# Optimization experiments

Measured on AMD Instinct MI355X. Metric: run time of the kernel, lower is better.

Reference implementation:

```python
import jax, jax.numpy as jnp
import numpy as np

B, HR, WR, C, HEADS, WS = 32, 64, 64, 128, 4, 8
HD = C // HEADS            # head dim = 32
N = WS * WS                # tokens per window = 64
NB = (2 * WS - 1) ** 2     # relative-bias table rows = 225
EPS = 1e-5


def _relative_bias_index():
    # Static int index, identical to SwinMSA._get_relative_bias_index
    coords = np.stack(np.meshgrid(np.arange(WS), np.arange(WS), indexing='ij'))  # (2, ws, ws)
    flat = coords.reshape(2, -1)                      # (2, n)
    rel = flat[:, :, None] - flat[:, None, :]         # (2, n, n)
    rel = rel.transpose(1, 2, 0).copy()               # (n, n, 2)
    rel[:, :, 0] += WS - 1
    rel[:, :, 1] += WS - 1
    rel[:, :, 0] *= 2 * WS - 1
    return rel.sum(-1)                                # (n, n) int

_REL_IDX = _relative_bias_index()


def _ln(x, g, b):
    m = jnp.mean(x, axis=-1, keepdims=True)
    v = jnp.mean(jnp.square(x - m), axis=-1, keepdims=True)
    return (x - m) * jax.lax.rsqrt(v + EPS) * g + b


def setup_inputs() -> dict:
    key = jax.random.key(0)
    ks = jax.random.split(key, 16)
    s = 0.02
    return {
        'x': jax.random.normal(ks[0], (B, HR * WR, C), jnp.float32),
        'qkv_w': jax.random.normal(ks[1], (C, 3 * C), jnp.float32) * s,
        'qkv_b': jnp.zeros((3 * C,), jnp.float32),
        'proj_w': jax.random.normal(ks[2], (C, C), jnp.float32) * s,
        'proj_b': jnp.zeros((C,), jnp.float32),
        'rel_bias_table': jax.random.normal(ks[3], (NB, HEADS), jnp.float32) * s,
        'ln1_g': jnp.ones((C,), jnp.float32),
        'ln1_b': jnp.zeros((C,), jnp.float32),
        'ln2_g': jnp.ones((C,), jnp.float32),
        'ln2_b': jnp.zeros((C,), jnp.float32),
        'mlp_w1': jax.random.normal(ks[4], (C, 4 * C), jnp.float32) * s,
        'mlp_b1': jnp.zeros((4 * C,), jnp.float32),
        'mlp_w2': jax.random.normal(ks[5], (4 * C, C), jnp.float32) * s,
        'mlp_b2': jnp.zeros((C,), jnp.float32),
    }


def reference(x, qkv_w, qkv_b, proj_w, proj_b, rel_bias_table,
              ln1_g, ln1_b, ln2_g, ln2_b, mlp_w1, mlp_b1, mlp_w2, mlp_b2):
    b = x.shape[0]
    hb, wb = HR // WS, WR // WS
    img = x.reshape(b, HR, WR, C)
    n1 = _ln(img, ln1_g, ln1_b)
    # window_partition: '(wy h) (wx w)' split puts window coord OUTER (strided windows),
    # faithful to the source rearrange.
    part = n1.reshape(b, WS, hb, WS, wb, C).transpose(0, 2, 4, 1, 3, 5)
    part = part.reshape(b * hb * wb, N, C)            # (Bw, n, c)
    qkv = part @ qkv_w + qkv_b                        # (Bw, n, 3c)
    # rearrange 'b n (h d c) -> d b n h c': channel factors as (head, 3, head_dim)
    qkv = qkv.reshape(-1, N, HEADS, 3, HD)
    q, k, v = qkv[..., 0, :], qkv[..., 1, :], qkv[..., 2, :]   # (Bw, n, h, hd)
    energy = jnp.einsum('bqhe,bkhe->bqhk', q, k) * (HD ** -0.5)
    bias = rel_bias_table[_REL_IDX.reshape(-1)].reshape(N, N, HEADS)
    bias = bias.transpose(2, 0, 1)                    # (h, n, n)
    energy = energy + bias.transpose(1, 0, 2)[None]   # broadcast as (q, h, k)
    attn = jax.nn.softmax(energy, axis=-1)
    out = jnp.einsum('bihv,bvhd->bihd', attn, v).reshape(-1, N, C)
    out = out @ proj_w + proj_b                       # (Bw, n, c)
    # window_reverse (inverse of the strided partition)
    rev = out.reshape(b, hb, wb, WS, WS, C).transpose(0, 3, 1, 4, 2, 5)
    rev = rev.reshape(b, HR * WR, C)
    msa = x + rev
    h2 = _ln(msa, ln2_g, ln2_b)
    mlp = jax.nn.gelu(h2 @ mlp_w1 + mlp_b1, approximate=False) @ mlp_w2 + mlp_b2
    return msa + mlp
```

## Files before the change

### kernel.cpp

```cpp
#include <hip/hip_runtime.h>
#include <hip/hip_bf16.h>
#include <hip/hip_fp16.h>

typedef __attribute__((ext_vector_type(4))) float f32x4;
typedef __attribute__((ext_vector_type(8))) short bf16x8;
typedef __attribute__((ext_vector_type(4))) short bf16x4;
typedef unsigned short u16;
typedef unsigned char u8;

__device__ __forceinline__ short fbf(float f){
  __hip_bfloat16 h = __float2bfloat16(f);
  return *reinterpret_cast<short*>(&h);
}
__device__ __forceinline__ float bf2f(short s){
  return __uint_as_float(((unsigned)(unsigned short)s) << 16);
}
__device__ __forceinline__ unsigned f2e5(float v){
  __half h = __float2half(v);
  unsigned hu = (unsigned)*reinterpret_cast<unsigned short*>(&h);
  hu = hu + 0x7Fu + ((hu >> 8) & 1u);
  return (hu >> 8) & 0xFFu;
}
__device__ __forceinline__ float e52f(unsigned b){
  unsigned short hb = (unsigned short)(b << 8);
  __half h = *reinterpret_cast<__half*>(&hb);
  return __half2float(h);
}

#define LOG2E 1.4426950408889634f

__global__ void repack_kernel(const float* __restrict__ qkv_w, const float* __restrict__ proj_w,
                              const float* __restrict__ w1, const float* __restrict__ w2,
                              const float* __restrict__ tbl,
                              u16* __restrict__ rq, u16* __restrict__ rp,
                              u16* __restrict__ r1, u16* __restrict__ r2,
                              float* __restrict__ be){
  const int i = blockIdx.x * 256 + threadIdx.x;
  const int j = i & 7, lane = (i >> 3) & 63, f = i >> 9;
  const int kr = (lane >> 4) * 8 + j;
  const int c16 = lane & 15;
  if (i < 49152){ int nt = f % 24, kk = f / 24; rq[i] = (u16)fbf(qkv_w[(kk*32 + kr)*384 + nt*16 + c16]); }
  if (i < 16384){ int nt = f & 7,  kk = f >> 3; rp[i] = (u16)fbf(proj_w[(kk*32 + kr)*128 + nt*16 + c16]); }
  if (i < 65536){ int nt = f & 31, kk = f >> 5; r1[i] = (u16)fbf(w1[(kk*32 + kr)*512 + nt*16 + c16]); }
  if (i < 65536){ int nt = f & 7,  kk = f >> 3; r2[i] = (u16)fbf(w2[(kk*32 + kr)*128 + nt*16 + c16]); }
  if (i < 16384){
    int rg = i & 3, ln = (i >> 2) & 63, g = i >> 8;
    int nt = g & 3, mt = (g >> 2) & 3, h = g >> 4;
    int row = mt*16 + (ln >> 4)*4 + rg;
    int col = nt*16 + (ln & 15);
    int rel = ((col >> 3) - (row >> 3) + 7) * 15 + ((col & 7) - (row & 7) + 7);
    be[i] = tbl[rel*4 + h] * LOG2E;
  }
}

__global__ __launch_bounds__(256, 3)
void block_kernel(const float* __restrict__ x,
                  const float* __restrict__ qkv_b, const float* __restrict__ proj_b,
                  const float* __restrict__ ln1_g, const float* __restrict__ ln1_b,
                  const float* __restrict__ ln2_g, const float* __restrict__ ln2_b,
                  const u16* __restrict__ rep_qkv, const u16* __restrict__ rep_proj,
                  const u16* __restrict__ rep_w1, const u16* __restrict__ rep_w2,
                  const float* __restrict__ mlp_b1, const float* __restrict__ mlp_b2,
                  const float* __restrict__ bias_exp,
                  float* __restrict__ out){
  __shared__ __align__(16) u16 smem[20480];
  u16* sLN = smem;
  u16* sQ  = smem;
  u16* sK  = smem + 8192;
  u16* sP  = smem;
  u16* sO  = smem;
  u16* stg = smem + 8192;
  u16* sH  = smem;
  u16* sG  = smem + 16384;
  u8*  sVe5 = (u8*)(smem + 16384);

  const int tid = threadIdx.x, lane = tid & 63, wid = tid >> 6;
  const int wdw = blockIdx.x;
  const int bb = wdw >> 6, ihb = (wdw >> 3) & 7, iwb = wdw & 7;
  const float* xb = x + (size_t)bb * 4096 * 128;
  float* ob = out + (size_t)bb * 4096 * 128;
  const f32x4 z4 = {0.f, 0.f, 0.f, 0.f};
  const int rb = tid >> 4, cb = tid & 15, c0g = cb * 8;
  const int r15 = lane & 15, kg = lane >> 4;

  {
    float g8[8], b8[8];
    *(f32x4*)&g8[0] = *(const f32x4*)(ln1_g + c0g);
    *(f32x4*)&g8[4] = *(const f32x4*)(ln1_g + c0g + 4);
    *(f32x4*)&b8[0] = *(const f32x4*)(ln1_b + c0g);
    *(f32x4*)&b8[4] = *(const f32x4*)(ln1_b + c0g + 4);
    #pragma unroll
    for (int it = 0; it < 4; ++it){
      const int r = it * 16 + rb;
      const int pix = ((r >> 3) * 8 + ihb) * 64 + (r & 7) * 8 + iwb;
      float fl[8];
      *(f32x4*)&fl[0] = *(const f32x4*)(xb + (size_t)pix * 128 + c0g);
      *(f32x4*)&fl[4] = *(const f32x4*)(xb + (size_t)pix * 128 + c0g + 4);
      float s = 0.f, sq = 0.f;
      #pragma unroll
      for (int j = 0; j < 8; ++j){ s += fl[j]; sq += fl[j]*fl[j]; }
      #pragma unroll
      for (int m = 1; m < 16; m <<= 1){ s += __shfl_xor(s, m); sq += __shfl_xor(sq, m); }
      const float mean = s * (1.f/128.f);
      const float rs = __builtin_amdgcn_rsqf(sq * (1.f/128.f) - mean*mean + 1e-5f);
      bf16x8 o;
      #pragma unroll
      for (int j = 0; j < 8; ++j) o[j] = fbf((fl[j]-mean)*rs*g8[j] + b8[j]);
      *(bf16x8*)&sLN[r*128 + (c0g ^ ((r & 7) << 3))] = o;
    }
  }
  __syncthreads();

  {
    f32x4 aqk[4][4];
    f32x4 av[4][2];
    #pragma unroll
    for (int ct = 0; ct < 4; ++ct){
      const f32x4 bq = *(const f32x4*)(qkv_b + wid*96 + ct*16 + kg*4);
      #pragma unroll
      for (int tt = 0; tt < 4; ++tt) aqk[ct][tt] = bq;
    }
    #pragma unroll
    for (int nt = 0; nt < 2; ++nt){
      const float bv = qkv_b[wid*96 + 64 + nt*16 + r15];
      const f32x4 bv4 = {bv, bv, bv, bv};
      #pragma unroll
      for (int mt = 0; mt < 4; ++mt) av[mt][nt] = bv4;
    }
    #pragma unroll
    for (int kk = 0; kk < 4; ++kk){
      bf16x8 L[4], aW[4], bWv[2];
      const int c0 = kk*32 + kg*8;
      #pragma unroll
      for (int t = 0; t < 4; ++t){
        const int row = t*16 + r15;
        L[t] = *(const bf16x8*)&sLN[row*128 + (c0 ^ ((row & 7) << 3))];
      }
      #pragma unroll
      for (int ct = 0; ct < 4; ++ct)
        aW[ct] = *(const bf16x8*)(rep_qkv + (size_t)((kk*24 + wid*6 + ct)*64 + lane)*8);
      #pragma unroll
      for (int nt = 0; nt < 2; ++nt)
        bWv[nt] = *(const bf16x8*)(rep_qkv + (size_t)((kk*24 + wid*6 + 4 + nt)*64 + lane)*8);
      #pragma unroll
      for (int ct = 0; ct < 4; ++ct)
        #pragma unroll
        for (int tt = 0; tt < 4; ++tt)
          aqk[ct][tt] = __builtin_amdgcn_mfma_f32_16x16x32_bf16(aW[ct], L[tt], aqk[ct][tt], 0, 0, 0);
      #pragma unroll
      for (int mt = 0; mt < 4; ++mt)
        #pragma unroll
        for (int nt = 0; nt < 2; ++nt)
          av[mt][nt] = __builtin_amdgcn_mfma_f32_16x16x32_bf16(L[mt], bWv[nt], av[mt][nt], 0, 0, 0);
    }
    __syncthreads();
    #pragma unroll
    for (int ct = 0; ct < 4; ++ct){
      u16* dst = (ct < 2) ? sQ : sK;
      const float scl = (ct < 2) ? 0.2550348296f : 1.0f;
      const int colu = wid*32 + (ct & 1)*16 + kg*4;
      #pragma unroll
      for (int tt = 0; tt < 4; ++tt){
        const int row = tt*16 + r15;
        bf16x4 pk;
        #pragma unroll
        for (int rg = 0; rg < 4; ++rg) pk[rg] = fbf(aqk[ct][tt][rg] * scl);
        *(bf16x4*)&dst[row*128 + (colu ^ ((row & 7) << 3))] = pk;
      }
    }
    #pragma unroll
    for (int nt = 0; nt < 2; ++nt){
      const int row = wid*32 + nt*16 + r15;
      #pragma unroll
      for (int mt = 0; mt < 4; ++mt){
        const int colu = mt*16 + kg*4;
        unsigned pk = f2e5(av[mt][nt][0]) | (f2e5(av[mt][nt][1]) << 8)
                    | (f2e5(av[mt][nt][2]) << 16) | (f2e5(av[mt][nt][3]) << 24);
        *(unsigned*)(sVe5 + row*64 + (colu ^ ((row & 7) << 3))) = pk;
      }
    }
  }
  __syncthreads();

  f32x4 s4[4][4];
  {
    bf16x8 aK[4], bQ[4];
    #pragma unroll
    for (int t = 0; t < 4; ++t){
      const int row = t*16 + r15;
      const int off = (wid*32 + kg*8) ^ ((row & 7) << 3);
      aK[t] = *(const bf16x8*)&sK[row*128 + off];
      bQ[t] = *(const bf16x8*)&sQ[row*128 + off];
    }
    #pragma unroll
    for (int mtk = 0; mtk < 4; ++mtk)
      #pragma unroll
      for (int ntq = 0; ntq < 4; ++ntq){
        const f32x4 cb4 = *(const f32x4*)(bias_exp + (size_t)(((wid*4 + mtk)*4 + ntq)*64 + lane)*4);
        s4[mtk][ntq] = __builtin_amdgcn_mfma_f32_16x16x32_bf16(aK[mtk], bQ[ntq], cb4, 0, 0, 0);
      }
  }
  #pragma unroll
  for (int ntq = 0; ntq < 4; ++ntq){
    float sum = 0.f;
    #pragma unroll
    for (int mtk = 0; mtk < 4; ++mtk)
      #pragma unroll
      for (int rg = 0; rg < 4; ++rg){
        const float e = __builtin_amdgcn_exp2f(s4[mtk][ntq][rg]);
        s4[mtk][ntq][rg] = e; sum += e;
      }
    sum += __shfl_xor(sum, 16);
    sum += __shfl_xor(sum, 32);
    const float inv = __builtin_amdgcn_rcpf(sum);
    #pragma unroll
    for (int mtk = 0; mtk < 4; ++mtk)
      #pragma unroll
      for (int rg = 0; rg < 4; ++rg) s4[mtk][ntq][rg] *= inv;
  }
  __syncthreads();
  #pragma unroll
  for (int ntq = 0; ntq < 4; ++ntq){
    const int row = ntq*16 + r15;
    #pragma unroll
    for (int mtk = 0; mtk < 4; ++mtk){
      const int colu = mtk*16 + kg*4;
      bf16x4 pk;
      #pragma unroll
      for (int rg = 0; rg < 4; ++rg) pk[rg] = fbf(s4[mtk][ntq][rg]);
      *(bf16x4*)&sP[wid*4096 + row*64 + (colu ^ ((row & 7) << 3))] = pk;
    }
  }

  {
    f32x4 o4[2][4];
    #pragma unroll
    for (int dt = 0; dt < 2; ++dt)
      #pragma unroll
      for (int qt = 0; qt < 4; ++qt) o4[dt][qt] = z4;
    #pragma unroll
    for (int ks = 0; ks < 2; ++ks){
      bf16x8 aV[2], bP[4];
      #pragma unroll
      for (int dt = 0; dt < 2; ++dt){
        const int rowd = wid*32 + dt*16 + r15;
        const u8* pv = sVe5 + rowd*64 + ((ks*32 + kg*8) ^ ((rowd & 7) << 3));
        const unsigned w0 = *(const unsigned*)pv;
        const unsigned w1 = *(const unsigned*)(pv + 4);
        bf16x8 a;
        #pragma unroll
        for (int j = 0; j < 4; ++j){
          a[j]   = fbf(e52f((w0 >> (8*j)) & 0xFFu));
          a[4+j] = fbf(e52f((w1 >> (8*j)) & 0xFFu));
        }
        aV[dt] = a;
      }
      #pragma unroll
      for (int qt = 0; qt < 4; ++qt){
        const int rowq = qt*16 + r15;
        bP[qt] = *(const bf16x8*)&sP[wid*4096 + rowq*64 + ((ks*32 + kg*8) ^ ((rowq & 7) << 3))];
      }
      #pragma unroll
      for (int dt = 0; dt < 2; ++dt)
        #pragma unroll
        for (int qt = 0; qt < 4; ++qt)
          o4[dt][qt] = __builtin_amdgcn_mfma_f32_16x16x32_bf16(aV[dt], bP[qt], o4[dt][qt], 0, 0, 0);
    }
    __syncthreads();
    #pragma unroll
    for (int dt = 0; dt < 2; ++dt){
      const int dbase = wid*32 + dt*16 + kg*4;
      #pragma unroll
      for (int qt = 0; qt < 4; ++qt){
        const int q = qt*16 + r15;
        bf16x4 pk;
        #pragma unroll
        for (int rg = 0; rg < 4; ++rg) pk[rg] = fbf(o4[dt][qt][rg]);
        *(bf16x4*)&sO[q*128 + (dbase ^ ((q & 7) << 3))] = pk;
      }
    }
  }
  __syncthreads();

  {
    f32x4 xv[2][4];
    #pragma unroll
    for (int ot = 0; ot < 2; ++ot){
      const int cbase = (wid*2 + ot)*16 + kg*4;
      #pragma unroll
      for (int tt = 0; tt < 4; ++tt){
        const int tok = tt*16 + r15;
        const int pix = ((tok >> 3) * 8 + ihb) * 64 + (tok & 7) * 8 + iwb;
        xv[ot][tt] = *(const f32x4*)(xb + (size_t)pix * 128 + cbase);
      }
    }
    f32x4 po[2][4];
    #pragma unroll
    for (int ot = 0; ot < 2; ++ot){
      const f32x4 pb4 = *(const f32x4*)(proj_b + (wid*2 + ot)*16 + kg*4);
      #pragma unroll
      for (int tt = 0; tt < 4; ++tt) po[ot][tt] = pb4;
    }
    #pragma unroll
    for (int kk = 0; kk < 4; ++kk){
      bf16x8 aWp[2], bO[4];
      #pragma unroll
      for (int ot = 0; ot < 2; ++ot)
        aWp[ot] = *(const bf16x8*)(rep_proj + (size_t)((kk*8 + wid*2 + ot)*64 + lane)*8);
      #pragma unroll
      for (int tt = 0; tt < 4; ++tt){
        const int row = tt*16 + r15;
        bO[tt] = *(const bf16x8*)&sO[row*128 + ((kk*32 + kg*8) ^ ((row & 7) << 3))];
      }
      #pragma unroll
      for (int ot = 0; ot < 2; ++ot)
        #pragma unroll
        for (int tt = 0; tt < 4; ++tt)
          po[ot][tt] = __builtin_amdgcn_mfma_f32_16x16x32_bf16(aWp[ot], bO[tt], po[ot][tt], 0, 0, 0);
    }
    #pragma unroll
    for (int ot = 0; ot < 2; ++ot){
      const int cbase = (wid*2 + ot)*16 + kg*4;
      #pragma unroll
      for (int tt = 0; tt < 4; ++tt){
        const int tok = tt*16 + r15;
        bf16x4 pk;
        #pragma unroll
        for (int rg = 0; rg < 4; ++rg) pk[rg] = fbf(po[ot][tt][rg] + xv[ot][tt][rg]);
        *(bf16x4*)&stg[tok*128 + (cbase ^ ((tok & 7) << 3))] = pk;
      }
    }
  }
  __syncthreads();

  {
    float g8[8], b8[8];
    *(f32x4*)&g8[0] = *(const f32x4*)(ln2_g + c0g);
    *(f32x4*)&g8[4] = *(const f32x4*)(ln2_g + c0g + 4);
    *(f32x4*)&b8[0] = *(const f32x4*)(ln2_b + c0g);
    *(f32x4*)&b8[4] = *(const f32x4*)(ln2_b + c0g + 4);
    #pragma unroll
    for (int it = 0; it < 4; ++it){
      const int r = it * 16 + rb;
      bf16x8 m8 = *(const bf16x8*)&stg[r*128 + (c0g ^ ((r & 7) << 3))];
      float fl[8];
      #pragma unroll
      for (int j = 0; j < 8; ++j) fl[j] = bf2f(m8[j]);
      float s = 0.f, sq = 0.f;
      #pragma unroll
      for (int j = 0; j < 8; ++j){ s += fl[j]; sq += fl[j]*fl[j]; }
      #pragma unroll
      for (int m = 1; m < 16; m <<= 1){ s += __shfl_xor(s, m); sq += __shfl_xor(sq, m); }
      const float mean = s * (1.f/128.f);
      const float rs = __builtin_amdgcn_rsqf(sq * (1.f/128.f) - mean*mean + 1e-5f);
      bf16x8 o;
      #pragma unroll
      for (int j = 0; j < 8; ++j) o[j] = fbf((fl[j]-mean)*rs*g8[j] + b8[j]);
      *(bf16x8*)&sH[r*128 + (c0g ^ ((r & 7) << 3))] = o;
    }
  }
  __syncthreads();

  f32x4 accO[2][4];
  #pragma unroll
  for (int ot = 0; ot < 2; ++ot){
    const f32x4 b2v = *(const f32x4*)(mlp_b2 + (wid*2 + ot)*16 + kg*4);
    #pragma unroll
    for (int tt = 0; tt < 4; ++tt) accO[ot][tt] = b2v;
  }
  #pragma unroll
  for (int c = 0; c < 8; ++c){
    f32x4 t4[4];
    {
      const f32x4 b1v = *(const f32x4*)(mlp_b1 + c*64 + wid*16 + kg*4);
      #pragma unroll
      for (int tt = 0; tt < 4; ++tt) t4[tt] = b1v;
    }
    #pragma unroll
    for (int kk = 0; kk < 4; ++kk){
      const int c0 = kk*32 + kg*8;
      bf16x8 aW = *(const bf16x8*)(rep_w1 + (size_t)((kk*32 + c*4 + wid)*64 + lane)*8);
      bf16x8 bL[4];
      #pragma unroll
      for (int tt = 0; tt < 4; ++tt){
        const int row = tt*16 + r15;
        bL[tt] = *(const bf16x8*)&sH[row*128 + (c0 ^ ((row & 7) << 3))];
      }
      #pragma unroll
      for (int tt = 0; tt < 4; ++tt)
        t4[tt] = __builtin_amdgcn_mfma_f32_16x16x32_bf16(aW, bL[tt], t4[tt], 0, 0, 0);
    }
    bf16x4 gp[4];
    #pragma unroll
    for (int tt = 0; tt < 4; ++tt){
      #pragma unroll
      for (int rg = 0; rg < 4; ++rg){
        const float v = t4[tt][rg];
        const float e = __builtin_amdgcn_exp2f(-2.4554669f * v);
        gp[tt][rg] = fbf(v * __builtin_amdgcn_rcpf(1.f + e));
      }
    }
    __syncthreads();
    {
      const int colu = wid*16 + kg*4;
      #pragma unroll
      for (int tt = 0; tt < 4; ++tt){
        const int row = tt*16 + r15;
        *(bf16x4*)&sG[row*64 + (colu ^ ((row & 7) << 3))] = gp[tt];
      }
    }
    __syncthreads();
    #pragma unroll
    for (int kk2 = 0; kk2 < 2; ++kk2){
      bf16x8 aW2[2], bG[4];
      const int c0 = kk2*32 + kg*8;
      #pragma unroll
      for (int ot = 0; ot < 2; ++ot)
        aW2[ot] = *(const bf16x8*)(rep_w2 + (size_t)(((c*2 + kk2)*8 + wid*2 + ot)*64 + lane)*8);
      #pragma unroll
      for (int tt = 0; tt < 4; ++tt){
        const int row = tt*16 + r15;
        bG[tt] = *(const bf16x8*)&sG[row*64 + (c0 ^ ((row & 7) << 3))];
      }
      #pragma unroll
      for (int ot = 0; ot < 2; ++ot)
        #pragma unroll
        for (int tt = 0; tt < 4; ++tt)
          accO[ot][tt] = __builtin_amdgcn_mfma_f32_16x16x32_bf16(aW2[ot], bG[tt], accO[ot][tt], 0, 0, 0);
    }
  }

  #pragma unroll
  for (int ot = 0; ot < 2; ++ot){
    const int cbase = (wid*2 + ot)*16 + kg*4;
    #pragma unroll
    for (int tt = 0; tt < 4; ++tt){
      const int tok = tt*16 + r15;
      const int pix = ((tok >> 3) * 8 + ihb) * 64 + (tok & 7) * 8 + iwb;
      bf16x4 m4 = *(const bf16x4*)&stg[tok*128 + (cbase ^ ((tok & 7) << 3))];
      f32x4 o;
      #pragma unroll
      for (int rg = 0; rg < 4; ++rg) o[rg] = bf2f(m4[rg]) + accO[ot][tt][rg];
      *(f32x4*)(ob + (size_t)pix * 128 + cbase) = o;
    }
  }
}

extern "C" void kernel_launch(void* const* d_in, const int* in_sizes, int n_in,
                              void* d_out, int out_size, void* d_ws, size_t ws_size,
                              hipStream_t stream){
  (void)in_sizes; (void)n_in; (void)out_size; (void)ws_size;
  const float* x      = (const float*)d_in[0];
  const float* qkv_w  = (const float*)d_in[1];
  const float* qkv_b  = (const float*)d_in[2];
  const float* proj_w = (const float*)d_in[3];
  const float* proj_b = (const float*)d_in[4];
  const float* tbl    = (const float*)d_in[5];
  const float* ln1_g  = (const float*)d_in[6];
  const float* ln1_b  = (const float*)d_in[7];
  const float* ln2_g  = (const float*)d_in[8];
  const float* ln2_b  = (const float*)d_in[9];
  const float* w1     = (const float*)d_in[10];
  const float* b1     = (const float*)d_in[11];
  const float* w2     = (const float*)d_in[12];
  const float* b2     = (const float*)d_in[13];

  char* ws = (char*)d_ws;
  u16*   rq  = (u16*)ws;
  u16*   rp  = (u16*)(ws + 98304);
  u16*   r1  = (u16*)(ws + 131072);
  u16*   r2  = (u16*)(ws + 262144);
  float* be  = (float*)(ws + 393216);

  hipLaunchKernelGGL(repack_kernel, dim3(256), dim3(256), 0, stream,
                     qkv_w, proj_w, w1, w2, tbl, rq, rp, r1, r2, be);
  hipLaunchKernelGGL(block_kernel, dim3(2048), dim3(256), 0, stream,
                     x, qkv_b, proj_b, ln1_g, ln1_b, ln2_g, ln2_b,
                     rq, rp, r1, r2, b1, b2, be, (float*)d_out);
}
```

Measured before the change: 103.9 us.

## Split each window across eight waves by head and token half

Doubles the block size to 512 threads. Each of the eight waves now handles one head (or output column group) for half of the window's 64 tokens, where before one wave covered a head for all tokens. Per-wave accumulator and fragment arrays are halved, and launch bounds move from (256,3) to (512,2). This cuts register pressure and puts more waves in flight per CU. In exchange, each weight fragment is loaded from global memory by two waves instead of one, and each block synchronises more waves at every barrier.

```diff
diff --git a/kernel.cpp b/kernel.cpp
--- a/kernel.cpp
+++ b/kernel.cpp
@@ -53,7 +53,7 @@
   }
 }
 
-__global__ __launch_bounds__(256, 3)
+__global__ __launch_bounds__(512, 2)
 void block_kernel(const float* __restrict__ x,
                   const float* __restrict__ qkv_b, const float* __restrict__ proj_b,
                   const float* __restrict__ ln1_g, const float* __restrict__ ln1_b,
@@ -74,7 +74,8 @@
   u16* sG  = smem + 16384;
   u8*  sVe5 = (u8*)(smem + 16384);
 
-  const int tid = threadIdx.x, lane = tid & 63, wid = tid >> 6;
+  const int tid = threadIdx.x, lane = tid & 63, wid8 = tid >> 6;
+  const int head = wid8 & 3, half = wid8 >> 2, tb = half * 2;
   const int wdw = blockIdx.x;
   const int bb = wdw >> 6, ihb = (wdw >> 3) & 7, iwb = wdw & 7;
   const float* xb = x + (size_t)bb * 4096 * 128;
@@ -90,8 +91,8 @@
     *(f32x4*)&b8[0] = *(const f32x4*)(ln1_b + c0g);
     *(f32x4*)&b8[4] = *(const f32x4*)(ln1_b + c0g + 4);
     #pragma unroll
-    for (int it = 0; it < 4; ++it){
-      const int r = it * 16 + rb;
+    for (int it = 0; it < 2; ++it){
+      const int r = it * 32 + rb;
       const int pix = ((r >> 3) * 8 + ihb) * 64 + (r & 7) * 8 + iwb;
       float fl[8];
       *(f32x4*)&fl[0] = *(const f32x4*)(xb + (size_t)pix * 128 + c0g);
@@ -112,103 +113,106 @@
   __syncthreads();
 
   {
-    f32x4 aqk[4][4];
-    f32x4 av[4][2];
+    f32x4 aqk[4][2];
+    f32x4 av[2][2];
     #pragma unroll
     for (int ct = 0; ct < 4; ++ct){
-      const f32x4 bq = *(const f32x4*)(qkv_b + wid*96 + ct*16 + kg*4);
-      #pragma unroll
-      for (int tt = 0; tt < 4; ++tt) aqk[ct][tt] = bq;
+      const f32x4 bq = *(const f32x4*)(qkv_b + head*96 + ct*16 + kg*4);
+      #pragma unroll
+      for (int t2 = 0; t2 < 2; ++t2) aqk[ct][t2] = bq;
     }
     #pragma unroll
     for (int nt = 0; nt < 2; ++nt){
-      const float bv = qkv_b[wid*96 + 64 + nt*16 + r15];
+      const float bv = qkv_b[head*96 + 64 + nt*16 + r15];
       const f32x4 bv4 = {bv, bv, bv, bv};
       #pragma unroll
-      for (int mt = 0; mt < 4; ++mt) av[mt][nt] = bv4;
+      for (int t2 = 0; t2 < 2; ++t2) av[t2][nt] = bv4;
     }
     #pragma unroll
     for (int kk = 0; kk < 4; ++kk){
-      bf16x8 L[4], aW[4], bWv[2];
+      bf16x8 L[2], aW[4], bWv[2];
       const int c0 = kk*32 + kg*8;
       #pragma unroll
-      for (int t = 0; t < 4; ++t){
-        const int row = t*16 + r15;
-        L[t] = *(const bf16x8*)&sLN[row*128 + (c0 ^ ((row & 7) << 3))];
+      for (int t2 = 0; t2 < 2; ++t2){
+        const int row = (tb + t2)*16 + r15;
+        L[t2] = *(const bf16x8*)&sLN[row*128 + (c0 ^ ((row & 7) << 3))];
       }
       #pragma unroll
       for (int ct = 0; ct < 4; ++ct)
-        aW[ct] = *(const bf16x8*)(rep_qkv + (size_t)((kk*24 + wid*6 + ct)*64 + lane)*8);
+        aW[ct] = *(const bf16x8*)(rep_qkv + (size_t)((kk*24 + head*6 + ct)*64 + lane)*8);
       #pragma unroll
       for (int nt = 0; nt < 2; ++nt)
-        bWv[nt] = *(const bf16x8*)(rep_qkv + (size_t)((kk*24 + wid*6 + 4 + nt)*64 + lane)*8);
+        bWv[nt] = *(const bf16x8*)(rep_qkv + (size_t)((kk*24 + head*6 + 4 + nt)*64 + lane)*8);
       #pragma unroll
       for (int ct = 0; ct < 4; ++ct)
         #pragma unroll
-        for (int tt = 0; tt < 4; ++tt)
-          aqk[ct][tt] = __builtin_amdgcn_mfma_f32_16x16x32_bf16(aW[ct], L[tt], aqk[ct][tt], 0, 0, 0);
-      #pragma unroll
-      for (int mt = 0; mt < 4; ++mt)
+        for (int t2 = 0; t2 < 2; ++t2)
+          aqk[ct][t2] = __builtin_amdgcn_mfma_f32_16x16x32_bf16(aW[ct], L[t2], aqk[ct][t2], 0, 0, 0);
+      #pragma unroll
+      for (int t2 = 0; t2 < 2; ++t2)
         #pragma unroll
         for (int nt = 0; nt < 2; ++nt)
-          av[mt][nt] = __builtin_amdgcn_mfma_f32_16x16x32_bf16(L[mt], bWv[nt], av[mt][nt], 0, 0, 0);
+          av[t2][nt] = __builtin_amdgcn_mfma_f32_16x16x32_bf16(L[t2], bWv[nt], av[t2][nt], 0, 0, 0);
     }
     __syncthreads();
     #pragma unroll
     for (int ct = 0; ct < 4; ++ct){
       u16* dst = (ct < 2) ? sQ : sK;
       const float scl = (ct < 2) ? 0.2550348296f : 1.0f;
-      const int colu = wid*32 + (ct & 1)*16 + kg*4;
-      #pragma unroll
-      for (int tt = 0; tt < 4; ++tt){
-        const int row = tt*16 + r15;
+      const int colu = head*32 + (ct & 1)*16 + kg*4;
+      #pragma unroll
+      for (int t2 = 0; t2 < 2; ++t2){
+        const int row = (tb + t2)*16 + r15;
         bf16x4 pk;
         #pragma unroll
-        for (int rg = 0; rg < 4; ++rg) pk[rg] = fbf(aqk[ct][tt][rg] * scl);
+        for (int rg = 0; rg < 4; ++rg) pk[rg] = fbf(aqk[ct][t2][rg] * scl);
         *(bf16x4*)&dst[row*128 + (colu ^ ((row & 7) << 3))] = pk;
       }
     }
     #pragma unroll
     for (int nt = 0; nt < 2; ++nt){
-      const int row = wid*32 + nt*16 + r15;
-      #pragma unroll
-      for (int mt = 0; mt < 4; ++mt){
-        const int colu = mt*16 + kg*4;
-        unsigned pk = f2e5(av[mt][nt][0]) | (f2e5(av[mt][nt][1]) << 8)
-                    | (f2e5(av[mt][nt][2]) << 16) | (f2e5(av[mt][nt][3]) << 24);
+      const int row = head*32 + nt*16 + r15;
+      #pragma unroll
+      for (int t2 = 0; t2 < 2; ++t2){
+        const int colu = (tb + t2)*16 + kg*4;
+        unsigned pk = f2e5(av[t2][nt][0]) | (f2e5(av[t2][nt][1]) << 8)
+                    | (f2e5(av[t2][nt][2]) << 16) | (f2e5(av[t2][nt][3]) << 24);
         *(unsigned*)(sVe5 + row*64 + (colu ^ ((row & 7) << 3))) = pk;
       }
     }
   }
   __syncthreads();
 
-  f32x4 s4[4][4];
-  {
-    bf16x8 aK[4], bQ[4];
+  f32x4 s4[4][2];
+  {
+    bf16x8 aK[4], bQ[2];
     #pragma unroll
     for (int t = 0; t < 4; ++t){
       const int row = t*16 + r15;
-      const int off = (wid*32 + kg*8) ^ ((row & 7) << 3);
-      aK[t] = *(const bf16x8*)&sK[row*128 + off];
-      bQ[t] = *(const bf16x8*)&sQ[row*128 + off];
+      aK[t] = *(const bf16x8*)&sK[row*128 + ((head*32 + kg*8) ^ ((row & 7) << 3))];
+    }
+    #pragma unroll
+    for (int q2 = 0; q2 < 2; ++q2){
+      const int row = (tb + q2)*16 + r15;
+      bQ[q2] = *(const bf16x8*)&sQ[row*128 + ((head*32 + kg*8) ^ ((row & 7) << 3))];
     }
     #pragma unroll
     for (int mtk = 0; mtk < 4; ++mtk)
       #pragma unroll
-      for (int ntq = 0; ntq < 4; ++ntq){
-        const f32x4 cb4 = *(const f32x4*)(bias_exp + (size_t)(((wid*4 + mtk)*4 + ntq)*64 + lane)*4);
-        s4[mtk][ntq] = __builtin_amdgcn_mfma_f32_16x16x32_bf16(aK[mtk], bQ[ntq], cb4, 0, 0, 0);
+      for (int q2 = 0; q2 < 2; ++q2){
+        const f32x4 cb4 = *(const f32x4*)(bias_exp + (size_t)(((head*4 + mtk)*4 + tb + q2)*64 + lane)*4);
+        s4[mtk][q2] = __builtin_amdgcn_mfma_f32_16x16x32_bf16(aK[mtk], bQ[q2], cb4, 0, 0, 0);
       }
   }
   #pragma unroll
-  for (int ntq = 0; ntq < 4; ++ntq){
+  for (int q2 = 0; q2 < 2; ++q2){
     float sum = 0.f;
     #pragma unroll
     for (int mtk = 0; mtk < 4; ++mtk)
       #pragma unroll
       for (int rg = 0; rg < 4; ++rg){
-        const float e = __builtin_amdgcn_exp2f(s4[mtk][ntq][rg]);
-        s4[mtk][ntq][rg] = e; sum += e;
+        const float e = __builtin_amdgcn_exp2f(s4[mtk][q2][rg]);
+        s4[mtk][q2][rg] = e; sum += e;
       }
     sum += __shfl_xor(sum, 16);
     sum += __shfl_xor(sum, 32);
@@ -216,34 +220,34 @@
     #pragma unroll
     for (int mtk = 0; mtk < 4; ++mtk)
       #pragma unroll
-      for (int rg = 0; rg < 4; ++rg) s4[mtk][ntq][rg] *= inv;
+      for (int rg = 0; rg < 4; ++rg) s4[mtk][q2][rg] *= inv;
   }
   __syncthreads();
   #pragma unroll
-  for (int ntq = 0; ntq < 4; ++ntq){
-    const int row = ntq*16 + r15;
+  for (int q2 = 0; q2 < 2; ++q2){
+    const int row = (tb + q2)*16 + r15;
     #pragma unroll
     for (int mtk = 0; mtk < 4; ++mtk){
       const int colu = mtk*16 + kg*4;
       bf16x4 pk;
       #pragma unroll
-      for (int rg = 0; rg < 4; ++rg) pk[rg] = fbf(s4[mtk][ntq][rg]);
-      *(bf16x4*)&sP[wid*4096 + row*64 + (colu ^ ((row & 7) << 3))] = pk;
-    }
-  }
-
-  {
-    f32x4 o4[2][4];
+      for (int rg = 0; rg < 4; ++rg) pk[rg] = fbf(s4[mtk][q2][rg]);
+      *(bf16x4*)&sP[head*4096 + row*64 + (colu ^ ((row & 7) << 3))] = pk;
+    }
+  }
+
+  {
+    f32x4 o4[2][2];
     #pragma unroll
     for (int dt = 0; dt < 2; ++dt)
       #pragma unroll
-      for (int qt = 0; qt < 4; ++qt) o4[dt][qt] = z4;
+      for (int q2 = 0; q2 < 2; ++q2) o4[dt][q2] = z4;
     #pragma unroll
     for (int ks = 0; ks < 2; ++ks){
-      bf16x8 aV[2], bP[4];
+      bf16x8 aV[2], bP[2];
       #pragma unroll
       for (int dt = 0; dt < 2; ++dt){
-        const int rowd = wid*32 + dt*16 + r15;
+        const int rowd = head*32 + dt*16 + r15;
         const u8* pv = sVe5 + rowd*64 + ((ks*32 + kg*8) ^ ((rowd & 7) << 3));
         const unsigned w0 = *(const unsigned*)pv;
         const unsigned w1 = *(const unsigned*)(pv + 4);
@@ -256,26 +260,26 @@
         aV[dt] = a;
       }
       #pragma unroll
-      for (int qt = 0; qt < 4; ++qt){
-        const int rowq = qt*16 + r15;
-        bP[qt] = *(const bf16x8*)&sP[wid*4096 + rowq*64 + ((ks*32 + kg*8) ^ ((rowq & 7) << 3))];
+      for (int q2 = 0; q2 < 2; ++q2){
+        const int rowq = (tb + q2)*16 + r15;
+        bP[q2] = *(const bf16x8*)&sP[head*4096 + rowq*64 + ((ks*32 + kg*8) ^ ((rowq & 7) << 3))];
       }
       #pragma unroll
       for (int dt = 0; dt < 2; ++dt)
         #pragma unroll
-        for (int qt = 0; qt < 4; ++qt)
-          o4[dt][qt] = __builtin_amdgcn_mfma_f32_16x16x32_bf16(aV[dt], bP[qt], o4[dt][qt], 0, 0, 0);
+        for (int q2 = 0; q2 < 2; ++q2)
+          o4[dt][q2] = __builtin_amdgcn_mfma_f32_16x16x32_bf16(aV[dt], bP[q2], o4[dt][q2], 0, 0, 0);
     }
     __syncthreads();
     #pragma unroll
     for (int dt = 0; dt < 2; ++dt){
-      const int dbase = wid*32 + dt*16 + kg*4;
-      #pragma unroll
-      for (int qt = 0; qt < 4; ++qt){
-        const int q = qt*16 + r15;
+      const int dbase = head*32 + dt*16 + kg*4;
+      #pragma unroll
+      for (int q2 = 0; q2 < 2; ++q2){
+        const int q = (tb + q2)*16 + r15;
         bf16x4 pk;
         #pragma unroll
-        for (int rg = 0; rg < 4; ++rg) pk[rg] = fbf(o4[dt][qt][rg]);
+        for (int rg = 0; rg < 4; ++rg) pk[rg] = fbf(o4[dt][q2][rg]);
         *(bf16x4*)&sO[q*128 + (dbase ^ ((q & 7) << 3))] = pk;
       }
     }
@@ -283,50 +287,50 @@
   __syncthreads();
 
   {
-    f32x4 xv[2][4];
+    f32x4 xv[2][2];
     #pragma unroll
     for (int ot = 0; ot < 2; ++ot){
-      const int cbase = (wid*2 + ot)*16 + kg*4;
-      #pragma unroll
-      for (int tt = 0; tt < 4; ++tt){
-        const int tok = tt*16 + r15;
+      const int cbase = (head*2 + ot)*16 + kg*4;
+      #pragma unroll
+      for (int t2 = 0; t2 < 2; ++t2){
+        const int tok = (tb + t2)*16 + r15;
         const int pix = ((tok >> 3) * 8 + ihb) * 64 + (tok & 7) * 8 + iwb;
-        xv[ot][tt] = *(const f32x4*)(xb + (size_t)pix * 128 + cbase);
-      }
-    }
-    f32x4 po[2][4];
+        xv[ot][t2] = *(const f32x4*)(xb + (size_t)pix * 128 + cbase);
+      }
+    }
+    f32x4 po[2][2];
     #pragma unroll
     for (int ot = 0; ot < 2; ++ot){
-      const f32x4 pb4 = *(const f32x4*)(proj_b + (wid*2 + ot)*16 + kg*4);
-      #pragma unroll
-      for (int tt = 0; tt < 4; ++tt) po[ot][tt] = pb4;
+      const f32x4 pb4 = *(const f32x4*)(proj_b + (head*2 + ot)*16 + kg*4);
+      #pragma unroll
+      for (int t2 = 0; t2 < 2; ++t2) po[ot][t2] = pb4;
     }
     #pragma unroll
     for (int kk = 0; kk < 4; ++kk){
-      bf16x8 aWp[2], bO[4];
+      bf16x8 aWp[2], bO[2];
       #pragma unroll
       for (int ot = 0; ot < 2; ++ot)
-        aWp[ot] = *(const bf16x8*)(rep_proj + (size_t)((kk*8 + wid*2 + ot)*64 + lane)*8);
-      #pragma unroll
-      for (int tt = 0; tt < 4; ++tt){
-        const int row = tt*16 + r15;
-        bO[tt] = *(const bf16x8*)&sO[row*128 + ((kk*32 + kg*8) ^ ((row & 7) << 3))];
+        aWp[ot] = *(const bf16x8*)(rep_proj + (size_t)((kk*8 + head*2 + ot)*64 + lane)*8);
+      #pragma unroll
+      for (int t2 = 0; t2 < 2; ++t2){
+        const int row = (tb + t2)*16 + r15;
+        bO[t2] = *(const bf16x8*)&sO[row*128 + ((kk*32 + kg*8) ^ ((row & 7) << 3))];
       }
       #pragma unroll
       for (int ot = 0; ot < 2; ++ot)
         #pragma unroll
-        for (int tt = 0; tt < 4; ++tt)
-          po[ot][tt] = __builtin_amdgcn_mfma_f32_16x16x32_bf16(aWp[ot], bO[tt], po[ot][tt], 0, 0, 0);
+        for (int t2 = 0; t2 < 2; ++t2)
+          po[ot][t2] = __builtin_amdgcn_mfma_f32_16x16x32_bf16(aWp[ot], bO[t2], po[ot][t2], 0, 0, 0);
     }
     #pragma unroll
     for (int ot = 0; ot < 2; ++ot){
-      const int cbase = (wid*2 + ot)*16 + kg*4;
-      #pragma unroll
-      for (int tt = 0; tt < 4; ++tt){
-        const int tok = tt*16 + r15;
+      const int cbase = (head*2 + ot)*16 + kg*4;
+      #pragma unroll
+      for (int t2 = 0; t2 < 2; ++t2){
+        const int tok = (tb + t2)*16 + r15;
         bf16x4 pk;
         #pragma unroll
-        for (int rg = 0; rg < 4; ++rg) pk[rg] = fbf(po[ot][tt][rg] + xv[ot][tt][rg]);
+        for (int rg = 0; rg < 4; ++rg) pk[rg] = fbf(po[ot][t2][rg] + xv[ot][t2][rg]);
         *(bf16x4*)&stg[tok*128 + (cbase ^ ((tok & 7) << 3))] = pk;
       }
     }
@@ -340,8 +344,8 @@
     *(f32x4*)&b8[0] = *(const f32x4*)(ln2_b + c0g);
     *(f32x4*)&b8[4] = *(const f32x4*)(ln2_b + c0g + 4);
     #pragma unroll
-    for (int it = 0; it < 4; ++it){
-      const int r = it * 16 + rb;
+    for (int it = 0; it < 2; ++it){
+      const int r = it * 32 + rb;
       bf16x8 m8 = *(const bf16x8*)&stg[r*128 + (c0g ^ ((r & 7) << 3))];
       float fl[8];
       #pragma unroll
@@ -361,86 +365,86 @@
   }
   __syncthreads();
 
-  f32x4 accO[2][4];
+  f32x4 accO[2][2];
   #pragma unroll
   for (int ot = 0; ot < 2; ++ot){
-    const f32x4 b2v = *(const f32x4*)(mlp_b2 + (wid*2 + ot)*16 + kg*4);
-    #pragma unroll
-    for (int tt = 0; tt < 4; ++tt) accO[ot][tt] = b2v;
+    const f32x4 b2v = *(const f32x4*)(mlp_b2 + (head*2 + ot)*16 + kg*4);
+    #pragma unroll
+    for (int t2 = 0; t2 < 2; ++t2) accO[ot][t2] = b2v;
   }
   #pragma unroll
   for (int c = 0; c < 8; ++c){
-    f32x4 t4[4];
+    f32x4 t4[2];
     {
-      const f32x4 b1v = *(const f32x4*)(mlp_b1 + c*64 + wid*16 + kg*4);
-      #pragma unroll
-      for (int tt = 0; tt < 4; ++tt) t4[tt] = b1v;
+      const f32x4 b1v = *(const f32x4*)(mlp_b1 + (c*4 + head)*16 + kg*4);
+      #pragma unroll
+      for (int t2 = 0; t2 < 2; ++t2) t4[t2] = b1v;
     }
     #pragma unroll
     for (int kk = 0; kk < 4; ++kk){
       const int c0 = kk*32 + kg*8;
-      bf16x8 aW = *(const bf16x8*)(rep_w1 + (size_t)((kk*32 + c*4 + wid)*64 + lane)*8);
-      bf16x8 bL[4];
-      #pragma unroll
-      for (int tt = 0; tt < 4; ++tt){
-        const int row = tt*16 + r15;
-        bL[tt] = *(const bf16x8*)&sH[row*128 + (c0 ^ ((row & 7) << 3))];
-      }
-      #pragma unroll
-      for (int tt = 0; tt < 4; ++tt)
-        t4[tt] = __builtin_amdgcn_mfma_f32_16x16x32_bf16(aW, bL[tt], t4[tt], 0, 0, 0);
-    }
-    bf16x4 gp[4];
-    #pragma unroll
-    for (int tt = 0; tt < 4; ++tt){
+      bf16x8 aW = *(const bf16x8*)(rep_w1 + (size_t)((kk*32 + c*4 + head)*64 + lane)*8);
+      bf16x8 bL[2];
+      #pragma unroll
+      for (int t2 = 0; t2 < 2; ++t2){
+        const int row = (tb + t2)*16 + r15;
+        bL[t2] = *(const bf16x8*)&sH[row*128 + (c0 ^ ((row & 7) << 3))];
+      }
+      #pragma unroll
+      for (int t2 = 0; t2 < 2; ++t2)
+        t4[t2] = __builtin_amdgcn_mfma_f32_16x16x32_bf16(aW, bL[t2], t4[t2], 0, 0, 0);
+    }
+    bf16x4 gp[2];
+    #pragma unroll
+    for (int t2 = 0; t2 < 2; ++t2){
       #pragma unroll
       for (int rg = 0; rg < 4; ++rg){
-        const float v = t4[tt][rg];
+        const float v = t4[t2][rg];
         const float e = __builtin_amdgcn_exp2f(-2.4554669f * v);
-        gp[tt][rg] = fbf(v * __builtin_amdgcn_rcpf(1.f + e));
+        gp[t2][rg] = fbf(v * __builtin_amdgcn_rcpf(1.f + e));
       }
     }
     __syncthreads();
     {
-      const int colu = wid*16 + kg*4;
-      #pragma unroll
-      for (int tt = 0; tt < 4; ++tt){
-        const int row = tt*16 + r15;
-        *(bf16x4*)&sG[row*64 + (colu ^ ((row & 7) << 3))] = gp[tt];
+      const int colu = head*16 + kg*4;
+      #pragma unroll
+      for (int t2 = 0; t2 < 2; ++t2){
+        const int row = (tb + t2)*16 + r15;
+        *(bf16x4*)&sG[row*64 + (colu ^ ((row & 7) << 3))] = gp[t2];
       }
     }
     __syncthreads();
     #pragma unroll
     for (int kk2 = 0; kk2 < 2; ++kk2){
-      bf16x8 aW2[2], bG[4];
+      bf16x8 aW2[2], bG[2];
       const int c0 = kk2*32 + kg*8;
       #pragma unroll
       for (int ot = 0; ot < 2; ++ot)
-        aW2[ot] = *(const bf16x8*)(rep_w2 + (size_t)(((c*2 + kk2)*8 + wid*2 + ot)*64 + lane)*8);
-      #pragma unroll
-      for (int tt = 0; tt < 4; ++tt){
-        const int row = tt*16 + r15;
-        bG[tt] = *(const bf16x8*)&sG[row*64 + (c0 ^ ((row & 7) << 3))];
+        aW2[ot] = *(const bf16x8*)(rep_w2 + (size_t)(((c*2 + kk2)*8 + head*2 + ot)*64 + lane)*8);
+      #pragma unroll
+      for (int t2 = 0; t2 < 2; ++t2){
+        const int row = (tb + t2)*16 + r15;
+        bG[t2] = *(const bf16x8*)&sG[row*64 + (c0 ^ ((row & 7) << 3))];
       }
       #pragma unroll
       for (int ot = 0; ot < 2; ++ot)
         #pragma unroll
-        for (int tt = 0; tt < 4; ++tt)
-          accO[ot][tt] = __builtin_amdgcn_mfma_f32_16x16x32_bf16(aW2[ot], bG[tt], accO[ot][tt], 0, 0, 0);
+        for (int t2 = 0; t2 < 2; ++t2)
+          accO[ot][t2] = __builtin_amdgcn_mfma_f32_16x16x32_bf16(aW2[ot], bG[t2], accO[ot][t2], 0, 0, 0);
     }
   }
 
   #pragma unroll
   for (int ot = 0; ot < 2; ++ot){
-    const int cbase = (wid*2 + ot)*16 + kg*4;
-    #pragma unroll
-    for (int tt = 0; tt < 4; ++tt){
-      const int tok = tt*16 + r15;
+    const int cbase = (head*2 + ot)*16 + kg*4;
+    #pragma unroll
+    for (int t2 = 0; t2 < 2; ++t2){
+      const int tok = (tb + t2)*16 + r15;
       const int pix = ((tok >> 3) * 8 + ihb) * 64 + (tok & 7) * 8 + iwb;
       bf16x4 m4 = *(const bf16x4*)&stg[tok*128 + (cbase ^ ((tok & 7) << 3))];
       f32x4 o;
       #pragma unroll
-      for (int rg = 0; rg < 4; ++rg) o[rg] = bf2f(m4[rg]) + accO[ot][tt][rg];
+      for (int rg = 0; rg < 4; ++rg) o[rg] = bf2f(m4[rg]) + accO[ot][t2][rg];
       *(f32x4*)(ob + (size_t)pix * 128 + cbase) = o;
     }
   }
@@ -474,7 +478,7 @@
 
   hipLaunchKernelGGL(repack_kernel, dim3(256), dim3(256), 0, stream,
                      qkv_w, proj_w, w1, w2, tbl, rq, rp, r1, r2, be);
-  hipLaunchKernelGGL(block_kernel, dim3(2048), dim3(256), 0, stream,
+  hipLaunchKernelGGL(block_kernel, dim3(2048), dim3(512), 0, stream,
                      x, qkv_b, proj_b, ln1_g, ln1_b, ln2_g, ln2_b,
                      rq, rp, r1, r2, b1, b2, be, (float*)d_out);
 }
```

Result: slower. 112.7 us (+8.5%).
